# Kernel tuning notes

Hardware: AMD Instinct MI355X
Metric: run time of the kernel (lower is better)

## Reference

```python
import jax, jax.numpy as jnp
import numpy as np

NEG_SLOPE = 0.2
N_NODES = 50000
N_EDGES = 800000
NUM_GRAPHS = 128
IN_F, HID_F, OUT_F = 64, 64, 64


def _gat_layer(x, src, dst, W, a_src, a_dst, b, n_nodes):
    # x: [N, Fin] -> out: [N, Fout]; single-head PyG GATConv with self-loops
    xp = x @ W                                   # [N, Fout]
    alpha_src = xp @ a_src                       # [N]
    alpha_dst = xp @ a_dst                       # [N]
    e = jax.nn.leaky_relu(alpha_src[src] + alpha_dst[dst], NEG_SLOPE)  # [E]
    # segment softmax over incoming edges of each dst node
    m = jax.ops.segment_max(e, dst, num_segments=n_nodes)
    ex = jnp.exp(e - m[dst])
    denom = jax.ops.segment_sum(ex, dst, num_segments=n_nodes)
    alpha = ex / denom[dst]                      # [E]
    out = jax.ops.segment_sum(alpha[:, None] * xp[src], dst, num_segments=n_nodes)
    return out + b


def setup_inputs() -> dict:
    key = jax.random.key(0)
    ks = jax.random.split(key, 12)
    x = jax.random.normal(ks[0], (N_NODES, IN_F), dtype=jnp.float32)
    edge_index = jax.random.randint(ks[1], (2, N_EDGES), 0, N_NODES, dtype=jnp.int64 if jax.config.jax_enable_x64 else jnp.int32)
    batch = jnp.sort(jax.random.randint(ks[2], (N_NODES,), 0, NUM_GRAPHS, dtype=edge_index.dtype))
    s = 0.1
    W1 = jax.random.normal(ks[3], (IN_F, HID_F), dtype=jnp.float32) * s
    att_src1 = jax.random.normal(ks[4], (HID_F,), dtype=jnp.float32) * s
    att_dst1 = jax.random.normal(ks[5], (HID_F,), dtype=jnp.float32) * s
    b1 = jax.random.normal(ks[6], (HID_F,), dtype=jnp.float32) * s
    W2 = jax.random.normal(ks[7], (HID_F, OUT_F), dtype=jnp.float32) * s
    att_src2 = jax.random.normal(ks[8], (OUT_F,), dtype=jnp.float32) * s
    att_dst2 = jax.random.normal(ks[9], (OUT_F,), dtype=jnp.float32) * s
    b2 = jax.random.normal(ks[10], (OUT_F,), dtype=jnp.float32) * s
    return {"x": x, "edge_index": edge_index, "batch": batch,
            "W1": W1, "att_src1": att_src1, "att_dst1": att_dst1, "b1": b1,
            "W2": W2, "att_src2": att_src2, "att_dst2": att_dst2, "b2": b2}


def reference(x, edge_index, batch, W1, att_src1, att_dst1, b1, W2, att_src2, att_dst2, b2):
    n = x.shape[0]
    # add self-loops (PyG GATConv default)
    loops = jnp.arange(n, dtype=edge_index.dtype)
    src = jnp.concatenate([edge_index[0], loops])
    dst = jnp.concatenate([edge_index[1], loops])
    h = _gat_layer(x, src, dst, W1, att_src1, att_dst1, b1, n)
    h = jax.nn.relu(h)  # dropout = identity at eval
    h = _gat_layer(h, src, dst, W2, att_src2, att_dst2, b2, n)
    h = jax.nn.relu(h)
    # scatter_mean over graphs
    sums = jax.ops.segment_sum(h, batch, num_segments=NUM_GRAPHS)
    counts = jax.ops.segment_sum(jnp.ones((n,), dtype=h.dtype), batch, num_segments=NUM_GRAPHS)
    return sums / jnp.maximum(counts, 1.0)[:, None]
```

## Files before the change

### kernel.cpp

```cpp
#include <hip/hip_runtime.h>
#include <hip/hip_fp16.h>

#define FEAT 64
#define BK   64
#define CAP  1536
#define MAXB 1024
#define SEPT 16

typedef _Float16 f16;
typedef __attribute__((ext_vector_type(8))) _Float16 f16x8;
typedef __attribute__((ext_vector_type(4))) float    f32x4;

struct GemmSm {
    union {
        struct { f16 Xs[64][72]; f16 Wt[64][72]; };
        float Cs[4][16][68];
    };
    float asl[64], adl[64];
};

__device__ __forceinline__ void gemm_tile(
    GemmSm& sm, int row0, const float* __restrict__ xin,
    const float* __restrict__ W, const float* __restrict__ avs,
    const float* __restrict__ avd, unsigned* __restrict__ xph,
    float* __restrict__ as_, float* __restrict__ ad_, int n)
{
    const int t = threadIdx.x;
    const int lane = t & 63;
    const int wave = t >> 6;

    if (t < 64) sm.asl[t] = avs[t];
    else if (t < 128) sm.adl[t - 64] = avd[t - 64];

    for (int i = t; i < 64 * 16; i += 256) {
        const int r = i >> 4, c4 = (i & 15) << 2;
        const int gr = row0 + r;
        float4 v = make_float4(0.f, 0.f, 0.f, 0.f);
        if (gr < n) v = *(const float4*)(xin + (size_t)gr * FEAT + c4);
        sm.Xs[r][c4 + 0] = (f16)v.x; sm.Xs[r][c4 + 1] = (f16)v.y;
        sm.Xs[r][c4 + 2] = (f16)v.z; sm.Xs[r][c4 + 3] = (f16)v.w;
    }
    for (int i = t; i < 64 * 16; i += 256) {
        const int k = i >> 4, c4 = (i & 15) << 2;
        const float4 v = *(const float4*)(W + k * FEAT + c4);
        sm.Wt[c4 + 0][k] = (f16)v.x; sm.Wt[c4 + 1][k] = (f16)v.y;
        sm.Wt[c4 + 2][k] = (f16)v.z; sm.Wt[c4 + 3][k] = (f16)v.w;
    }
    __syncthreads();

    const int mrow = (wave << 4) + (lane & 15);
    const int kg = lane >> 4;
    const f16x8 a0 = *(const f16x8*)(&sm.Xs[mrow][kg * 8]);
    const f16x8 a1 = *(const f16x8*)(&sm.Xs[mrow][32 + kg * 8]);

    f32x4 acc[4];
#pragma unroll
    for (int nt = 0; nt < 4; ++nt) {
        const int ncol = nt * 16 + (lane & 15);
        const f16x8 b0 = *(const f16x8*)(&sm.Wt[ncol][kg * 8]);
        const f16x8 b1 = *(const f16x8*)(&sm.Wt[ncol][32 + kg * 8]);
        f32x4 c = {0.f, 0.f, 0.f, 0.f};
        c = __builtin_amdgcn_mfma_f32_16x16x32_f16(a0, b0, c, 0, 0, 0);
        c = __builtin_amdgcn_mfma_f32_16x16x32_f16(a1, b1, c, 0, 0, 0);
        acc[nt] = c;
    }
    __syncthreads();

#pragma unroll
    for (int nt = 0; nt < 4; ++nt)
#pragma unroll
        for (int reg = 0; reg < 4; ++reg)
            sm.Cs[wave][(lane >> 4) * 4 + reg][nt * 16 + (lane & 15)] = acc[nt][reg];

    for (int i = lane; i < 16 * 32; i += 64) {
        const int r = i >> 5, fp = i & 31;
        const int node = row0 + (wave << 4) + r;
        if (node < n) {
            const __half2 pk = __floats2half2_rn(sm.Cs[wave][r][2 * fp],
                                                 sm.Cs[wave][r][2 * fp + 1]);
            xph[(size_t)node * 32 + fp] = *(const unsigned*)&pk;
        }
    }
    {
        const int r = lane >> 2, q = lane & 3;
        float s1 = 0.f, s2 = 0.f;
#pragma unroll
        for (int j = 0; j < 16; ++j) {
            const int c = q * 16 + j;
            const float v = sm.Cs[wave][r][c];
            s1 += v * sm.asl[c];
            s2 += v * sm.adl[c];
        }
        s1 += __shfl_xor(s1, 1); s1 += __shfl_xor(s1, 2);
        s2 += __shfl_xor(s2, 1); s2 += __shfl_xor(s2, 2);
        const int node = row0 + (wave << 4) + r;
        if (q == 0 && node < n) { as_[node] = s1; ad_[node] = s2; }
    }
}

__global__ __launch_bounds__(256) void scatter_gemm1_kernel(
    const int* __restrict__ src, const int* __restrict__ dst,
    int* __restrict__ bcur, unsigned* __restrict__ ebuf,
    const float* __restrict__ x, const float* __restrict__ W,
    const float* __restrict__ a_src, const float* __restrict__ a_dst,
    unsigned* __restrict__ xph, float* __restrict__ as_, float* __restrict__ ad_,
    int n, int E, int nbuck, int nchunks)
{
    __shared__ union {
        struct { int hist[MAXB]; int base[MAXB]; } s;
        GemmSm g;
    } sm;

    const int t = threadIdx.x;

    if (blockIdx.x < (unsigned)nchunks) {
        for (int i = t; i < nbuck; i += 256) sm.s.hist[i] = 0;
        __syncthreads();

        unsigned code[SEPT]; int bk[SEPT], rk[SEPT];
        const int e0 = blockIdx.x * (256 * SEPT) + t;
#pragma unroll
        for (int k = 0; k < SEPT; ++k) {
            const int e = e0 + k * 256;
            bk[k] = -1;
            if (e < E) {
                const int s_ = src[e], d = dst[e];
                bk[k] = d >> 6;
                code[k] = ((unsigned)s_ << 6) | (unsigned)(d & 63);
                rk[k] = atomicAdd(&sm.s.hist[bk[k]], 1);
            }
        }
        __syncthreads();
        for (int i = t; i < nbuck; i += 256) {
            const int hv = sm.s.hist[i];
            sm.s.base[i] = hv ? atomicAdd(&bcur[i], hv) : 0;
        }
        __syncthreads();
#pragma unroll
        for (int k = 0; k < SEPT; ++k) {
            if (bk[k] >= 0) {
                const int pos = sm.s.base[bk[k]] + rk[k];
                if (pos < CAP) ebuf[(size_t)bk[k] * CAP + pos] = code[k];
            }
        }
    } else {
        gemm_tile(sm.g, (blockIdx.x - nchunks) * 64, x, W, a_src, a_dst,
                  xph, as_, ad_, n);
    }
}

__device__ __forceinline__ void agg_phaseB_to(
    const unsigned* scode, const float* sw, const int* startsL,
    const float* adb, const float* __restrict__ as_,
    const uint4* __restrict__ xph4,
    const float* __restrict__ bias,
    float* __restrict__ hout, int hstride,
    int g0, int n)
{
    const int lane = threadIdx.x & 63;
    const int wave = threadIdx.x >> 6;
    const int np = lane >> 5;
    const int q  = (lane >> 3) & 3;
    const int fo = lane & 7;

    for (int pair = wave; pair < BK / 2; pair += 8) {
        const int node = pair * 2 + np;
        const int g = g0 + node;
        const int gc = (g < n) ? g : (n - 1);
        const int st = startsL[node], en = startsL[node + 1];

        float a[8] = {0.f, 0.f, 0.f, 0.f, 0.f, 0.f, 0.f, 0.f};
        float wsum = 0.f;

        int i = st + q;
        for (; i + 12 < en; i += 16) {
            const unsigned c0 = scode[i];
            const unsigned c1 = scode[i + 4];
            const unsigned c2 = scode[i + 8];
            const unsigned c3 = scode[i + 12];
            const float w0 = sw[i], w1 = sw[i + 4], w2 = sw[i + 8], w3 = sw[i + 12];
            const uint4 x0 = xph4[(size_t)(c0 >> 6) * 8 + fo];
            const uint4 x1 = xph4[(size_t)(c1 >> 6) * 8 + fo];
            const uint4 x2 = xph4[(size_t)(c2 >> 6) * 8 + fo];
            const uint4 x3 = xph4[(size_t)(c3 >> 6) * 8 + fo];
#pragma unroll
            for (int u = 0; u < 4; ++u) {
                const uint4 xv = (u == 0) ? x0 : (u == 1) ? x1 : (u == 2) ? x2 : x3;
                const float wv = (u == 0) ? w0 : (u == 1) ? w1 : (u == 2) ? w2 : w3;
                const __half2 p0 = *(const __half2*)&xv.x;
                const __half2 p1 = *(const __half2*)&xv.y;
                const __half2 p2 = *(const __half2*)&xv.z;
                const __half2 p3 = *(const __half2*)&xv.w;
                a[0] += wv * __low2float(p0);  a[1] += wv * __high2float(p0);
                a[2] += wv * __low2float(p1);  a[3] += wv * __high2float(p1);
                a[4] += wv * __low2float(p2);  a[5] += wv * __high2float(p2);
                a[6] += wv * __low2float(p3);  a[7] += wv * __high2float(p3);
            }
            wsum += (w0 + w1) + (w2 + w3);
        }
        for (; i < en; i += 4) {
            const unsigned c0 = scode[i];
            const float w0 = sw[i];
            const uint4 xv = xph4[(size_t)(c0 >> 6) * 8 + fo];
            const __half2 p0 = *(const __half2*)&xv.x;
            const __half2 p1 = *(const __half2*)&xv.y;
            const __half2 p2 = *(const __half2*)&xv.z;
            const __half2 p3 = *(const __half2*)&xv.w;
            a[0] += w0 * __low2float(p0);  a[1] += w0 * __high2float(p0);
            a[2] += w0 * __low2float(p1);  a[3] += w0 * __high2float(p1);
            a[4] += w0 * __low2float(p2);  a[5] += w0 * __high2float(p2);
            a[6] += w0 * __low2float(p3);  a[7] += w0 * __high2float(p3);
            wsum += w0;
        }

#pragma unroll
        for (int j = 0; j < 8; ++j) {
            a[j] += __shfl_xor(a[j], 8);
            a[j] += __shfl_xor(a[j], 16);
        }
        wsum += __shfl_xor(wsum, 8);
        wsum += __shfl_xor(wsum, 16);

        float tt = as_[gc] + adb[node];
        tt = (tt >= 0.f) ? tt : 0.2f * tt;
        const float wself = __expf(tt);
        const uint4 xg = xph4[(size_t)gc * 8 + fo];
        const __half2 s0 = *(const __half2*)&xg.x;
        const __half2 s1 = *(const __half2*)&xg.y;
        const __half2 s2 = *(const __half2*)&xg.z;
        const __half2 s3 = *(const __half2*)&xg.w;
        const float dinv = 1.f / (wsum + wself);
        const float4 bA = *(const float4*)(bias + 8 * fo);
        const float4 bB = *(const float4*)(bias + 8 * fo + 4);

        if (q == 0 && g < n) {
            float4 vA, vB;
            vA.x = fmaxf((a[0] + wself * __low2float(s0))  * dinv + bA.x, 0.f);
            vA.y = fmaxf((a[1] + wself * __high2float(s0)) * dinv + bA.y, 0.f);
            vA.z = fmaxf((a[2] + wself * __low2float(s1))  * dinv + bA.z, 0.f);
            vA.w = fmaxf((a[3] + wself * __high2float(s1)) * dinv + bA.w, 0.f);
            vB.x = fmaxf((a[4] + wself * __low2float(s2))  * dinv + bB.x, 0.f);
            vB.y = fmaxf((a[5] + wself * __high2float(s2)) * dinv + bB.y, 0.f);
            vB.z = fmaxf((a[6] + wself * __low2float(s3))  * dinv + bB.z, 0.f);
            vB.w = fmaxf((a[7] + wself * __high2float(s3)) * dinv + bB.w, 0.f);
            *(float4*)(hout + (size_t)node * hstride + 8 * fo)     = vA;
            *(float4*)(hout + (size_t)node * hstride + 8 * fo + 4) = vB;
        }
    }
}

__global__ __launch_bounds__(512) void sortagg1_gemm2_kernel(
    const int* __restrict__ bcur, unsigned* __restrict__ ebuf,
    int* __restrict__ startsG,
    const float* __restrict__ asA, const float* __restrict__ adA,
    const uint4* __restrict__ xphA, const float* __restrict__ b1,
    const float* __restrict__ W2, const float* __restrict__ asrc2,
    const float* __restrict__ adst2,
    unsigned* __restrict__ xphB, float* __restrict__ asB, float* __restrict__ adB,
    int n)
{
    __shared__ float htile[64][68];
    __shared__ union {
        struct { unsigned scode[CAP]; float sw[CAP]; int hist[BK]; int cur[BK]; } a;
        GemmSm g;
    } sm;
    __shared__ int starts[BK + 1];
    __shared__ float adb[BK];

    const int b = blockIdx.x;
    const int t = threadIdx.x;
    const int lane = t & 63, wave = t >> 6;
    const int g0 = b * BK;
    const int row0 = g0;

    if (t < BK) {
        sm.a.hist[t] = 0;
        adb[t] = (g0 + t < n) ? adA[g0 + t] : 0.f;
    }
    __syncthreads();

    int cnt = bcur[b];
    if (cnt > CAP) cnt = CAP;
    unsigned* eb = ebuf + (size_t)b * CAP;

    unsigned c[3];
#pragma unroll
    for (int k = 0; k < 3; ++k) {
        const int i = t + k * 512;
        if (i < cnt) { c[k] = eb[i]; atomicAdd(&sm.a.hist[c[k] & 63], 1); }
    }
    __syncthreads();
    if (wave == 0) {
        int v = sm.a.hist[lane];
#pragma unroll
        for (int o = 1; o < 64; o <<= 1) {
            const int u = __shfl_up(v, o);
            if (lane >= o) v += u;
        }
        starts[lane + 1] = v;
        sm.a.cur[lane] = v - sm.a.hist[lane];
        if (lane == 0) starts[0] = 0;
    }
    __syncthreads();
#pragma unroll
    for (int k = 0; k < 3; ++k) {
        const int i = t + k * 512;
        if (i < cnt) { const int p = atomicAdd(&sm.a.cur[c[k] & 63], 1); sm.a.scode[p] = c[k]; }
    }
    __syncthreads();

    unsigned cc[3]; float vv[3];
#pragma unroll
    for (int k = 0; k < 3; ++k) {
        const int i = t + k * 512;
        if (i < cnt) { cc[k] = sm.a.scode[i]; eb[i] = cc[k]; vv[k] = asA[cc[k] >> 6]; }
    }
    if (t <= BK) startsG[b * (BK + 1) + t] = starts[t];
#pragma unroll
    for (int k = 0; k < 3; ++k) {
        const int i = t + k * 512;
        if (i < cnt) {
            float tt = vv[k] + adb[cc[k] & 63];
            tt = (tt >= 0.f) ? tt : 0.2f * tt;
            sm.a.sw[i] = __expf(tt);
        }
    }
    __syncthreads();

    agg_phaseB_to(sm.a.scode, sm.a.sw, starts, adb, asA, xphA, b1,
                  &htile[0][0], 68, g0, n);
    __syncthreads();

    if (t < 64) sm.g.asl[t] = asrc2[t];
    else if (t < 128) sm.g.adl[t - 64] = adst2[t - 64];

    for (int i = t; i < 64 * 16; i += 512) {
        const int r = i >> 4, c4 = (i & 15) << 2;
        const float4 v = *(const float4*)(&htile[r][c4]);
        sm.g.Xs[r][c4 + 0] = (f16)v.x; sm.g.Xs[r][c4 + 1] = (f16)v.y;
        sm.g.Xs[r][c4 + 2] = (f16)v.z; sm.g.Xs[r][c4 + 3] = (f16)v.w;
    }
    for (int i = t; i < 64 * 16; i += 512) {
        const int k = i >> 4, c4 = (i & 15) << 2;
        const float4 v = *(const float4*)(W2 + k * FEAT + c4);
        sm.g.Wt[c4 + 0][k] = (f16)v.x; sm.g.Wt[c4 + 1][k] = (f16)v.y;
        sm.g.Wt[c4 + 2][k] = (f16)v.z; sm.g.Wt[c4 + 3][k] = (f16)v.w;
    }
    __syncthreads();

    f32x4 acc[4];
    if (wave < 4) {
        const int mrow = (wave << 4) + (lane & 15);
        const int kg = lane >> 4;
        const f16x8 a0 = *(const f16x8*)(&sm.g.Xs[mrow][kg * 8]);
        const f16x8 a1 = *(const f16x8*)(&sm.g.Xs[mrow][32 + kg * 8]);
#pragma unroll
        for (int nt = 0; nt < 4; ++nt) {
            const int ncol = nt * 16 + (lane & 15);
            const f16x8 b0 = *(const f16x8*)(&sm.g.Wt[ncol][kg * 8]);
            const f16x8 b1v = *(const f16x8*)(&sm.g.Wt[ncol][32 + kg * 8]);
            f32x4 cacc = {0.f, 0.f, 0.f, 0.f};
            cacc = __builtin_amdgcn_mfma_f32_16x16x32_f16(a0, b0, cacc, 0, 0, 0);
            cacc = __builtin_amdgcn_mfma_f32_16x16x32_f16(a1, b1v, cacc, 0, 0, 0);
            acc[nt] = cacc;
        }
    }
    __syncthreads();
    if (wave < 4) {
#pragma unroll
        for (int nt = 0; nt < 4; ++nt)
#pragma unroll
            for (int reg = 0; reg < 4; ++reg)
                sm.g.Cs[wave][(lane >> 4) * 4 + reg][nt * 16 + (lane & 15)] = acc[nt][reg];
    }
    __syncthreads();

    for (int i = t; i < 64 * 32; i += 512) {
        const int r = i >> 5, fp = i & 31;
        const int node = row0 + r;
        if (node < n) {
            const __half2 pk = __floats2half2_rn(sm.g.Cs[r >> 4][r & 15][2 * fp],
                                                 sm.g.Cs[r >> 4][r & 15][2 * fp + 1]);
            xphB[(size_t)node * 32 + fp] = *(const unsigned*)&pk;
        }
    }
    if (t < 256) {
        const int r = t >> 2, q = t & 3;
        float s1 = 0.f, s2 = 0.f;
#pragma unroll
        for (int j = 0; j < 16; ++j) {
            const int cidx = q * 16 + j;
            const float v = sm.g.Cs[r >> 4][r & 15][cidx];
            s1 += v * sm.g.asl[cidx];
            s2 += v * sm.g.adl[cidx];
        }
        s1 += __shfl_xor(s1, 1); s1 += __shfl_xor(s1, 2);
        s2 += __shfl_xor(s2, 1); s2 += __shfl_xor(s2, 2);
        const int node = row0 + r;
        if (q == 0 && node < n) { asB[node] = s1; adB[node] = s2; }
    }
}

__global__ __launch_bounds__(512) void agg2_kernel(
    const unsigned* __restrict__ ebuf, const int* __restrict__ startsG,
    const float* __restrict__ as_, const float* __restrict__ ad_,
    const uint4* __restrict__ xph4, const float* __restrict__ bias,
    float* __restrict__ h, int n)
{
    __shared__ unsigned scode[CAP];
    __shared__ float    sw[CAP];
    __shared__ int startsL[BK + 1];
    __shared__ float adb[BK];

    const int b = blockIdx.x;
    const int t = threadIdx.x;
    const int g0 = b * BK;

    if (t < BK) adb[t] = (g0 + t < n) ? ad_[g0 + t] : 0.f;
    if (t <= BK) startsL[t] = startsG[b * (BK + 1) + t];
    __syncthreads();

    const int cnt = startsL[BK];
    const unsigned* eb = ebuf + (size_t)b * CAP;

    unsigned cc[3]; float vv[3];
#pragma unroll
    for (int k = 0; k < 3; ++k) {
        const int i = t + k * 512;
        if (i < cnt) { cc[k] = eb[i]; vv[k] = as_[cc[k] >> 6]; }
    }
#pragma unroll
    for (int k = 0; k < 3; ++k) {
        const int i = t + k * 512;
        if (i < cnt) {
            float tt = vv[k] + adb[cc[k] & 63];
            tt = (tt >= 0.f) ? tt : 0.2f * tt;
            scode[i] = cc[k]; sw[i] = __expf(tt);
        }
    }
    __syncthreads();

    agg_phaseB_to(scode, sw, startsL, adb, as_, xph4, bias,
                  h + (size_t)g0 * FEAT, FEAT, g0, n);
}

__device__ __forceinline__ int lower_bound_i(const int* a, int n, int key)
{
    int lo = 0, hi = n;
    while (lo < hi) {
        const int mid = (lo + hi) >> 1;
        if (a[mid] < key) lo = mid + 1; else hi = mid;
    }
    return lo;
}

__global__ __launch_bounds__(256) void pool_kernel(
    const float* __restrict__ h, const int* __restrict__ batch,
    float* __restrict__ out, int n)
{
    const int g = blockIdx.x;
    const int lane = threadIdx.x & 63;
    const int wave = threadIdx.x >> 6;

    const int lo = lower_bound_i(batch, n, g);
    const int hi = lower_bound_i(batch, n, g + 1);

    float s0 = 0.f, s1 = 0.f, s2 = 0.f, s3 = 0.f;
    int i = lo + wave;
    for (; i + 12 < hi; i += 16) {
        s0 += h[(size_t)i * FEAT + lane];
        s1 += h[(size_t)(i + 4) * FEAT + lane];
        s2 += h[(size_t)(i + 8) * FEAT + lane];
        s3 += h[(size_t)(i + 12) * FEAT + lane];
    }
    for (; i < hi; i += 4)
        s0 += h[(size_t)i * FEAT + lane];
    const float sum = (s0 + s1) + (s2 + s3);

    __shared__ float part[4][FEAT];
    part[wave][lane] = sum;
    __syncthreads();
    if (wave == 0) {
        const float s = part[0][lane] + part[1][lane] + part[2][lane] + part[3][lane];
        out[(size_t)g * FEAT + lane] = s / fmaxf((float)(hi - lo), 1.f);
    }
}

extern "C" void kernel_launch(void* const* d_in, const int* in_sizes, int n_in,
                              void* d_out, int out_size, void* d_ws, size_t ws_size,
                              hipStream_t stream)
{
    const float* x      = (const float*)d_in[0];
    const int*   ei     = (const int*)d_in[1];
    const int*   batch  = (const int*)d_in[2];
    const float* W1     = (const float*)d_in[3];
    const float* asrc1  = (const float*)d_in[4];
    const float* adst1  = (const float*)d_in[5];
    const float* b1     = (const float*)d_in[6];
    const float* W2     = (const float*)d_in[7];
    const float* asrc2  = (const float*)d_in[8];
    const float* adst2  = (const float*)d_in[9];
    const float* b2     = (const float*)d_in[10];

    const int N = in_sizes[2];
    const int E = in_sizes[1] / 2;
    const int G = out_size / FEAT;

    const int* src = ei;
    const int* dst = ei + E;

    const int nbuck   = (N + BK - 1) / BK;
    const int nchunks = (E + 256 * SEPT - 1) / (256 * SEPT);
    const int gemmBlocks = (N + 63) / 64;

    unsigned* xphA    = (unsigned*)d_ws;
    unsigned* xphB    = xphA + (size_t)N * 32;
    float*    h       = (float*)(xphB + (size_t)N * 32);
    float*    asA     = h + (size_t)N * FEAT;
    float*    adA     = asA + N;
    float*    asB     = adA + N;
    float*    adB     = asB + N;
    int*      bcur    = (int*)(adB + N);
    unsigned* ebuf    = (unsigned*)(bcur + nbuck);
    int*      startsG = (int*)(ebuf + (size_t)nbuck * CAP);

    hipMemsetAsync(bcur, 0, (size_t)nbuck * sizeof(int), stream);
    scatter_gemm1_kernel<<<nchunks + gemmBlocks, 256, 0, stream>>>(
        src, dst, bcur, ebuf, x, W1, asrc1, adst1, xphA, asA, adA,
        N, E, nbuck, nchunks);
    sortagg1_gemm2_kernel<<<nbuck, 512, 0, stream>>>(
        bcur, ebuf, startsG, asA, adA, (const uint4*)xphA, b1,
        W2, asrc2, adst2, xphB, asB, adB, N);
    agg2_kernel<<<nbuck, 512, 0, stream>>>(ebuf, startsG, asB, adB,
                                           (const uint4*)xphB, b2, h, N);
    pool_kernel<<<G, 256, 0, stream>>>(h, batch, (float*)d_out, N);
}
```

Baseline: 181.5 us.

## Fuse graph mean-pooling into second aggregation kernel with per-block partial sums

The second GAT aggregation now accumulates relu outputs directly into per-block shared-memory partial sums for up to four consecutive graph ids, using atomics as a fallback for any others. This drops the N×64 intermediate h write and re-read. A light reduce kernel then combines the block partials and the atomic sums per graph. It adds shared memory and a zeroing pass to the aggregation kernel, which may lower occupancy.

```diff
diff --git a/kernel.cpp b/kernel.cpp
--- a/kernel.cpp
+++ b/kernel.cpp
@@ -6,6 +6,7 @@
 #define CAP  1536
 #define MAXB 1024
 #define SEPT 16
+#define LG   4
 
 typedef _Float16 f16;
 typedef __attribute__((ext_vector_type(8))) _Float16 f16x8;
@@ -152,10 +153,8 @@
 __device__ __forceinline__ void agg_phaseB_to(
     const unsigned* scode, const float* sw, const int* startsL,
     const float* adb, const float* __restrict__ as_,
-    const uint4* __restrict__ xph4,
-    const float* __restrict__ bias,
-    float* __restrict__ hout, int hstride,
-    int g0, int n)
+    const uint4* __restrict__ xph4, const float* __restrict__ bias,
+    float* __restrict__ hout, int hstride, int g0, int n)
 {
     const int lane = threadIdx.x & 63;
     const int wave = threadIdx.x >> 6;
@@ -401,23 +400,32 @@
     }
 }
 
-__global__ __launch_bounds__(512) void agg2_kernel(
+__global__ __launch_bounds__(512) void agg2_pool_kernel(
     const unsigned* __restrict__ ebuf, const int* __restrict__ startsG,
     const float* __restrict__ as_, const float* __restrict__ ad_,
     const uint4* __restrict__ xph4, const float* __restrict__ bias,
-    float* __restrict__ h, int n)
+    const int* __restrict__ batch, float* __restrict__ gpart,
+    float* __restrict__ osum, int n)
 {
     __shared__ unsigned scode[CAP];
     __shared__ float    sw[CAP];
     __shared__ int startsL[BK + 1];
     __shared__ float adb[BK];
+    __shared__ int batchL[BK];
+    __shared__ float gpartW[8][2][LG][FEAT];
 
     const int b = blockIdx.x;
     const int t = threadIdx.x;
+    const int lane = t & 63, wave = t >> 6;
     const int g0 = b * BK;
 
-    if (t < BK) adb[t] = (g0 + t < n) ? ad_[g0 + t] : 0.f;
+    if (t < BK) {
+        const int g = g0 + t;
+        adb[t] = (g < n) ? ad_[g] : 0.f;
+        batchL[t] = batch[(g < n) ? g : (n - 1)];
+    }
     if (t <= BK) startsL[t] = startsG[b * (BK + 1) + t];
+    for (int i = t; i < 8 * 2 * LG * FEAT; i += 512) ((float*)gpartW)[i] = 0.f;
     __syncthreads();
 
     const int cnt = startsL[BK];
@@ -440,8 +448,120 @@
     }
     __syncthreads();
 
-    agg_phaseB_to(scode, sw, startsL, adb, as_, xph4, bias,
-                  h + (size_t)g0 * FEAT, FEAT, g0, n);
+    const int np = lane >> 5;
+    const int q  = (lane >> 3) & 3;
+    const int fo = lane & 7;
+    const int gbase = batchL[0];
+
+    for (int pair = wave; pair < BK / 2; pair += 8) {
+        const int node = pair * 2 + np;
+        const int g = g0 + node;
+        const int gc = (g < n) ? g : (n - 1);
+        const int st = startsL[node], en = startsL[node + 1];
+
+        float a[8] = {0.f, 0.f, 0.f, 0.f, 0.f, 0.f, 0.f, 0.f};
+        float wsum = 0.f;
+
+        int i = st + q;
+        for (; i + 12 < en; i += 16) {
+            const unsigned c0 = scode[i];
+            const unsigned c1 = scode[i + 4];
+            const unsigned c2 = scode[i + 8];
+            const unsigned c3 = scode[i + 12];
+            const float w0 = sw[i], w1 = sw[i + 4], w2 = sw[i + 8], w3 = sw[i + 12];
+            const uint4 x0 = xph4[(size_t)(c0 >> 6) * 8 + fo];
+            const uint4 x1 = xph4[(size_t)(c1 >> 6) * 8 + fo];
+            const uint4 x2 = xph4[(size_t)(c2 >> 6) * 8 + fo];
+            const uint4 x3 = xph4[(size_t)(c3 >> 6) * 8 + fo];
+#pragma unroll
+            for (int u = 0; u < 4; ++u) {
+                const uint4 xv = (u == 0) ? x0 : (u == 1) ? x1 : (u == 2) ? x2 : x3;
+                const float wv = (u == 0) ? w0 : (u == 1) ? w1 : (u == 2) ? w2 : w3;
+                const __half2 p0 = *(const __half2*)&xv.x;
+                const __half2 p1 = *(const __half2*)&xv.y;
+                const __half2 p2 = *(const __half2*)&xv.z;
+                const __half2 p3 = *(const __half2*)&xv.w;
+                a[0] += wv * __low2float(p0);  a[1] += wv * __high2float(p0);
+                a[2] += wv * __low2float(p1);  a[3] += wv * __high2float(p1);
+                a[4] += wv * __low2float(p2);  a[5] += wv * __high2float(p2);
+                a[6] += wv * __low2float(p3);  a[7] += wv * __high2float(p3);
+            }
+            wsum += (w0 + w1) + (w2 + w3);
+        }
+        for (; i < en; i += 4) {
+            const unsigned c0 = scode[i];
+            const float w0 = sw[i];
+            const uint4 xv = xph4[(size_t)(c0 >> 6) * 8 + fo];
+            const __half2 p0 = *(const __half2*)&xv.x;
+            const __half2 p1 = *(const __half2*)&xv.y;
+            const __half2 p2 = *(const __half2*)&xv.z;
+            const __half2 p3 = *(const __half2*)&xv.w;
+            a[0] += w0 * __low2float(p0);  a[1] += w0 * __high2float(p0);
+            a[2] += w0 * __low2float(p1);  a[3] += w0 * __high2float(p1);
+            a[4] += w0 * __low2float(p2);  a[5] += w0 * __high2float(p2);
+            a[6] += w0 * __low2float(p3);  a[7] += w0 * __high2float(p3);
+            wsum += w0;
+        }
+
+#pragma unroll
+        for (int j = 0; j < 8; ++j) {
+            a[j] += __shfl_xor(a[j], 8);
+            a[j] += __shfl_xor(a[j], 16);
+        }
+        wsum += __shfl_xor(wsum, 8);
+        wsum += __shfl_xor(wsum, 16);
+
+        float tt = as_[gc] + adb[node];
+        tt = (tt >= 0.f) ? tt : 0.2f * tt;
+        const float wself = __expf(tt);
+        const uint4 xg = xph4[(size_t)gc * 8 + fo];
+        const __half2 s0 = *(const __half2*)&xg.x;
+        const __half2 s1 = *(const __half2*)&xg.y;
+        const __half2 s2 = *(const __half2*)&xg.z;
+        const __half2 s3 = *(const __half2*)&xg.w;
+        const float dinv = 1.f / (wsum + wself);
+        const float4 bA = *(const float4*)(bias + 8 * fo);
+        const float4 bB = *(const float4*)(bias + 8 * fo + 4);
+
+        if (q == 0 && g < n) {
+            float4 vA, vB;
+            vA.x = fmaxf((a[0] + wself * __low2float(s0))  * dinv + bA.x, 0.f);
+            vA.y = fmaxf((a[1] + wself * __high2float(s0)) * dinv + bA.y, 0.f);
+            vA.z = fmaxf((a[2] + wself * __low2float(s1))  * dinv + bA.z, 0.f);
+            vA.w = fmaxf((a[3] + wself * __high2float(s1)) * dinv + bA.w, 0.f);
+            vB.x = fmaxf((a[4] + wself * __low2float(s2))  * dinv + bB.x, 0.f);
+            vB.y = fmaxf((a[5] + wself * __high2float(s2)) * dinv + bB.y, 0.f);
+            vB.z = fmaxf((a[6] + wself * __low2float(s3))  * dinv + bB.z, 0.f);
+            vB.w = fmaxf((a[7] + wself * __high2float(s3)) * dinv + bB.w, 0.f);
+
+            const int lg = batchL[node] - gbase;
+            if (lg < LG) {
+                float* p = &gpartW[wave][np][lg][8 * fo];
+                float4 oA = *(float4*)p;
+                float4 oB = *(float4*)(p + 4);
+                oA.x += vA.x; oA.y += vA.y; oA.z += vA.z; oA.w += vA.w;
+                oB.x += vB.x; oB.y += vB.y; oB.z += vB.z; oB.w += vB.w;
+                *(float4*)p = oA;
+                *(float4*)(p + 4) = oB;
+            } else {
+                float* o = osum + (size_t)batchL[node] * FEAT + 8 * fo;
+                atomicAdd(o + 0, vA.x); atomicAdd(o + 1, vA.y);
+                atomicAdd(o + 2, vA.z); atomicAdd(o + 3, vA.w);
+                atomicAdd(o + 4, vB.x); atomicAdd(o + 5, vB.y);
+                atomicAdd(o + 6, vB.z); atomicAdd(o + 7, vB.w);
+            }
+        }
+    }
+    __syncthreads();
+
+    if (t < LG * FEAT) {
+        const int lg = t >> 6, f = t & 63;
+        float s = 0.f;
+#pragma unroll
+        for (int w = 0; w < 8; ++w)
+            s += gpartW[w][0][lg][f] + gpartW[w][1][lg][f];
+        gpart[((size_t)b * LG + lg) * FEAT + f] = s;
+    }
 }
 
 __device__ __forceinline__ int lower_bound_i(const int* a, int n, int key)
@@ -454,36 +574,27 @@
     return lo;
 }
 
-__global__ __launch_bounds__(256) void pool_kernel(
-    const float* __restrict__ h, const int* __restrict__ batch,
-    float* __restrict__ out, int n)
+__global__ __launch_bounds__(64) void pool_reduce_kernel(
+    const float* __restrict__ gpart, const float* __restrict__ osum,
+    const int* __restrict__ batch, float* __restrict__ out, int n, int G)
 {
     const int g = blockIdx.x;
-    const int lane = threadIdx.x & 63;
-    const int wave = threadIdx.x >> 6;
+    const int lane = threadIdx.x;
 
     const int lo = lower_bound_i(batch, n, g);
     const int hi = lower_bound_i(batch, n, g + 1);
 
-    float s0 = 0.f, s1 = 0.f, s2 = 0.f, s3 = 0.f;
-    int i = lo + wave;
-    for (; i + 12 < hi; i += 16) {
-        s0 += h[(size_t)i * FEAT + lane];
-        s1 += h[(size_t)(i + 4) * FEAT + lane];
-        s2 += h[(size_t)(i + 8) * FEAT + lane];
-        s3 += h[(size_t)(i + 12) * FEAT + lane];
-    }
-    for (; i < hi; i += 4)
-        s0 += h[(size_t)i * FEAT + lane];
-    const float sum = (s0 + s1) + (s2 + s3);
-
-    __shared__ float part[4][FEAT];
-    part[wave][lane] = sum;
-    __syncthreads();
-    if (wave == 0) {
-        const float s = part[0][lane] + part[1][lane] + part[2][lane] + part[3][lane];
-        out[(size_t)g * FEAT + lane] = s / fmaxf((float)(hi - lo), 1.f);
-    }
+    float s = osum[(size_t)g * FEAT + lane];
+    if (lo < hi) {
+        const int b0 = lo >> 6, b1 = (hi - 1) >> 6;
+        for (int b = b0; b <= b1; ++b) {
+            const int base = batch[b << 6];
+            const int lg = g - base;
+            if (lg >= 0 && lg < LG)
+                s += gpart[((size_t)b * LG + lg) * FEAT + lane];
+        }
+    }
+    out[(size_t)g * FEAT + lane] = s / fmaxf((float)(hi - lo), 1.f);
 }
 
 extern "C" void kernel_launch(void* const* d_in, const int* in_sizes, int n_in,
@@ -515,23 +626,28 @@
 
     unsigned* xphA    = (unsigned*)d_ws;
     unsigned* xphB    = xphA + (size_t)N * 32;
-    float*    h       = (float*)(xphB + (size_t)N * 32);
-    float*    asA     = h + (size_t)N * FEAT;
+    float*    asA     = (float*)(xphB + (size_t)N * 32);
     float*    adA     = asA + N;
     float*    asB     = adA + N;
     float*    adB     = asB + N;
     int*      bcur    = (int*)(adB + N);
-    unsigned* ebuf    = (unsigned*)(bcur + nbuck);
+    float*    osum    = (float*)(bcur + nbuck);
+    unsigned* ebuf    = (unsigned*)(osum + (size_t)G * FEAT);
     int*      startsG = (int*)(ebuf + (size_t)nbuck * CAP);
-
-    hipMemsetAsync(bcur, 0, (size_t)nbuck * sizeof(int), stream);
+    float*    gpart   = (float*)(startsG + nbuck * (BK + 1));
+
+    hipMemsetAsync(bcur, 0,
+                   (size_t)nbuck * sizeof(int) + (size_t)G * FEAT * sizeof(float),
+                   stream);
     scatter_gemm1_kernel<<<nchunks + gemmBlocks, 256, 0, stream>>>(
         src, dst, bcur, ebuf, x, W1, asrc1, adst1, xphA, asA, adA,
         N, E, nbuck, nchunks);
     sortagg1_gemm2_kernel<<<nbuck, 512, 0, stream>>>(
         bcur, ebuf, startsG, asA, adA, (const uint4*)xphA, b1,
         W2, asrc2, adst2, xphB, asB, adB, N);
-    agg2_kernel<<<nbuck, 512, 0, stream>>>(ebuf, startsG, asB, adB,
-                                           (const uint4*)xphB, b2, h, N);
-    pool_kernel<<<G, 256, 0, stream>>>(h, batch, (float*)d_out, N);
-}
+    agg2_pool_kernel<<<nbuck, 512, 0, stream>>>(
+        ebuf, startsG, asB, adB, (const uint4*)xphB, b2,
+        batch, gpart, osum, N);
+    pool_reduce_kernel<<<G, 64, 0, stream>>>(gpart, osum, batch,
+                                             (float*)d_out, N, G);
+}
```

After: 176.8 us. 1.03x faster.
